# Performance work log

Hardware: AMD Instinct MI355X
Metric: run time of the kernel (lower is better)

The kernel has to match this reference:

```python
import jax, jax.numpy as jnp
import numpy as np

B, L, D = 2, 4096, 128      # batch, seq_len, d_model
ED = 2 * D                  # d_inner (expand=2) = 256
N = 16                      # d_state
K = 4                       # d_conv
R = (D + 15) // 16          # dt_rank = 8
H = 2 * D                   # mlp hidden = 256


def setup_inputs() -> dict:
    key = jax.random.key(0)
    ks = jax.random.split(key, 20)
    s = 0.05
    inp = {
        "x": jax.random.normal(ks[0], (B, L, D), dtype=jnp.float32),
        # outer block LayerNorm (norm1)
        "norm1_g": jnp.ones((D,), jnp.float32),
        "norm1_b": jnp.zeros((D,), jnp.float32),
        # MambaLayer inner LayerNorm
        "inner_g": jnp.ones((D,), jnp.float32),
        "inner_b": jnp.zeros((D,), jnp.float32),
        # Mamba params
        "in_w": jax.random.normal(ks[1], (2 * ED, D), jnp.float32) * s,      # in_proj (no bias)
        "conv_w": jax.random.normal(ks[2], (ED, 1, K), jnp.float32) * s,     # depthwise conv
        "conv_b": jax.random.normal(ks[3], (ED,), jnp.float32) * s,
        "xproj_w": jax.random.normal(ks[4], (R + 2 * N, ED), jnp.float32) * s,  # x_proj (no bias)
        "dt_w": jax.random.normal(ks[5], (ED, R), jnp.float32) * s,
        "dt_b": jax.random.normal(ks[6], (ED,), jnp.float32) * s,
        "A_log": jnp.tile(jnp.log(jnp.arange(1, N + 1, dtype=jnp.float32)), (ED, 1)),  # [ED,N]
        "Dp": jnp.ones((ED,), jnp.float32),
        "out_w": jax.random.normal(ks[7], (D, ED), jnp.float32) * s,         # out_proj (no bias)
        # MLP
        "fc1_w": jax.random.normal(ks[8], (H, D), jnp.float32) * s,
        "fc1_b": jnp.zeros((H,), jnp.float32),
        "fc2_w": jax.random.normal(ks[9], (D, H), jnp.float32) * s,
        "fc2_b": jnp.zeros((D,), jnp.float32),
    }
    return inp


def _ln(x, g, b, eps=1e-5):
    m = jnp.mean(x, axis=-1, keepdims=True)
    v = jnp.mean((x - m) ** 2, axis=-1, keepdims=True)
    return (x - m) * jax.lax.rsqrt(v + eps) * g + b


def _mamba(x, in_w, conv_w, conv_b, xproj_w, dt_w, dt_b, A_log, Dp, out_w):
    # x: [B, L, D]
    xz = jnp.einsum('bld,ed->ble', x, in_w)          # [B,L,2*ED]
    u, z = jnp.split(xz, 2, axis=-1)                 # each [B,L,ED]
    # causal depthwise conv1d over L
    u_c = jnp.transpose(u, (0, 2, 1))                # [B,ED,L]
    u_c = jax.lax.conv_general_dilated(
        u_c, conv_w, window_strides=(1,), padding=[(K - 1, 0)],
        dimension_numbers=('NCH', 'OIH', 'NCH'), feature_group_count=ED)
    u = jax.nn.silu(jnp.transpose(u_c, (0, 2, 1)) + conv_b)   # [B,L,ED]
    # input-dependent dt, B, C
    dbc = jnp.einsum('ble,re->blr', u, xproj_w)      # [B,L,R+2N]
    dt, Bm, Cm = jnp.split(dbc, [R, R + N], axis=-1)
    delta = jax.nn.softplus(jnp.einsum('blr,er->ble', dt, dt_w) + dt_b)  # [B,L,ED]
    A = -jnp.exp(A_log)                              # [ED,N]
    deltaA = jnp.exp(jnp.einsum('ble,en->blen', delta, A))               # [B,L,ED,N]
    deltaBu = jnp.einsum('ble,bln,ble->blen', delta, Bm, u)              # [B,L,ED,N]
    # selective scan over L
    def step(h, inp):
        dA, dBu, Ct = inp                            # [B,ED,N],[B,ED,N],[B,N]
        h = dA * h + dBu
        y = jnp.einsum('ben,bn->be', h, Ct)
        return h, y
    h0 = jnp.zeros((B, ED, N), u.dtype)
    xs = (jnp.transpose(deltaA, (1, 0, 2, 3)),
          jnp.transpose(deltaBu, (1, 0, 2, 3)),
          jnp.transpose(Cm, (1, 0, 2)))
    _, ys = jax.lax.scan(step, h0, xs)               # [L,B,ED]
    y = jnp.transpose(ys, (1, 0, 2)) + u * Dp        # [B,L,ED]
    y = y * jax.nn.silu(z)
    return jnp.einsum('ble,de->bld', y, out_w)       # [B,L,D]


def reference(x, norm1_g, norm1_b, inner_g, inner_b, in_w, conv_w, conv_b,
              xproj_w, dt_w, dt_b, A_log, Dp, out_w, fc1_w, fc1_b, fc2_w, fc2_b):
    # attn branch: mamba(inner_LN(norm1(x)))
    a = _mamba(_ln(_ln(x, norm1_g, norm1_b), inner_g, inner_b),
               in_w, conv_w, conv_b, xproj_w, dt_w, dt_b, A_log, Dp, out_w)
    x = x + a
    # mlp branch (note: original applies norm1 again to updated x)
    h = _ln(x, norm1_g, norm1_b)
    h = jax.nn.gelu(jnp.einsum('bld,hd->blh', h, fc1_w) + fc1_b, approximate=False)
    h = jnp.einsum('blh,dh->bld', h, fc2_w) + fc2_b
    return x + h
```

## Files before the change

kernel.cpp:

```cpp
#include <hip/hip_runtime.h>
#include <hip/hip_bf16.h>
#include <math.h>

#define BB 2
#define LL 4096
#define DD 128
#define ED 256
#define NN 16
#define KK 4
#define RR 8
#define HH 256
#define NT (BB*LL)
#define NC 128
#define LC 32

#define LOG2E 1.4426950408889634f

typedef __attribute__((ext_vector_type(8))) short short8;
typedef __attribute__((ext_vector_type(8))) unsigned short ushort8v;
typedef __attribute__((ext_vector_type(4))) float floatx4;

__device__ __forceinline__ unsigned short f2bf(float f) {
  unsigned int b = __builtin_bit_cast(unsigned int, f);
  b += 0x7FFFu + ((b >> 16) & 1u);
  return (unsigned short)(b >> 16);
}

__device__ __forceinline__ float exp2_fast(float x) {
#if __has_builtin(__builtin_amdgcn_exp2f)
  return __builtin_amdgcn_exp2f(x);
#else
  return exp2f(x);
#endif
}

__device__ __forceinline__ ushort8v pack8(const float4& v0, const float4& v1) {
  ushort8v p;
  p[0]=f2bf(v0.x); p[1]=f2bf(v0.y); p[2]=f2bf(v0.z); p[3]=f2bf(v0.w);
  p[4]=f2bf(v1.x); p[5]=f2bf(v1.y); p[6]=f2bf(v1.z); p[7]=f2bf(v1.w);
  return p;
}

__global__ __launch_bounds__(256) void scan1g_k(
    const float* __restrict__ x,
    const float* __restrict__ g1, const float* __restrict__ b1,
    const float* __restrict__ g2, const float* __restrict__ b2,
    const float* __restrict__ in_w,
    const float* __restrict__ cw, const float* __restrict__ cb,
    const float* __restrict__ xpw,
    const float* __restrict__ dtw, const float* __restrict__ dtb,
    const float* __restrict__ A_log,
    float* __restrict__ uc, float* __restrict__ dbc,
    float* __restrict__ delta, float* __restrict__ gate,
    float* __restrict__ cA, float* __restrict__ cH) {
  __shared__ __align__(16) unsigned char SM[69776];
  auto Atile = reinterpret_cast<unsigned short(*)[136]>(SM);
  auto Wch   = reinterpret_cast<unsigned short(*)[136]>(SM);
  auto As    = reinterpret_cast<unsigned short(*)[264]>(SM);
  auto sdel  = reinterpret_cast<float(*)[128]>(SM);
  auto ubuf  = reinterpret_cast<float(*)[257]>(SM + 17408);
  auto Bs    = reinterpret_cast<unsigned short(*)[264]>(SM + 17408);
  auto sdbc  = reinterpret_cast<float(*)[40]>(SM + 17408);
  auto sus   = reinterpret_cast<float(*)[128]>(SM + 53392);

  const int eb = blockIdx.x, c = blockIdx.y, b = blockIdx.z;
  const int tid = threadIdx.x;
  const int t0 = b*LL + c*LC;
  const int wave = tid >> 6, lane = tid & 63;
  const int quad = lane >> 4, l16 = lane & 15;

  {
    const int lr = tid >> 2, lk = (tid & 3) * 32;
    if (lr < 48) {
      if (lr < 35 && !(c == 0 && lr < 3)) {
        const float* Ap = x + (size_t)(t0 - 3 + lr)*DD + lk;
        float4 av[8];
        float s = 0.f, sq = 0.f;
        #pragma unroll
        for (int g = 0; g < 8; g++) {
          av[g] = *(const float4*)(Ap + g*4);
          s  += av[g].x + av[g].y + av[g].z + av[g].w;
          sq += av[g].x*av[g].x + av[g].y*av[g].y + av[g].z*av[g].z + av[g].w*av[g].w;
        }
        s += __shfl_xor(s, 1);  s += __shfl_xor(s, 2);
        sq += __shfl_xor(sq, 1); sq += __shfl_xor(sq, 2);
        const float m1 = s * (1.f/128.f);
        const float rs1 = rsqrtf(sq*(1.f/128.f) - m1*m1 + 1e-5f);
        float s2 = 0.f, sq2 = 0.f;
        #pragma unroll
        for (int g = 0; g < 8; g++) {
          const float4 gg = *(const float4*)(g1 + lk + g*4);
          const float4 bb = *(const float4*)(b1 + lk + g*4);
          av[g].x = (av[g].x - m1)*rs1*gg.x + bb.x;
          av[g].y = (av[g].y - m1)*rs1*gg.y + bb.y;
          av[g].z = (av[g].z - m1)*rs1*gg.z + bb.z;
          av[g].w = (av[g].w - m1)*rs1*gg.w + bb.w;
          s2  += av[g].x + av[g].y + av[g].z + av[g].w;
          sq2 += av[g].x*av[g].x + av[g].y*av[g].y + av[g].z*av[g].z + av[g].w*av[g].w;
        }
        s2 += __shfl_xor(s2, 1);  s2 += __shfl_xor(s2, 2);
        sq2 += __shfl_xor(sq2, 1); sq2 += __shfl_xor(sq2, 2);
        const float m2 = s2 * (1.f/128.f);
        const float rs2 = rsqrtf(sq2*(1.f/128.f) - m2*m2 + 1e-5f);
        #pragma unroll
        for (int g = 0; g < 4; g++) {
          const float4 ga = *(const float4*)(g2 + lk + g*8);
          const float4 gb = *(const float4*)(g2 + lk + g*8 + 4);
          const float4 ba = *(const float4*)(b2 + lk + g*8);
          const float4 bbv= *(const float4*)(b2 + lk + g*8 + 4);
          ushort8v pa;
          pa[0] = f2bf((av[2*g].x   - m2)*rs2*ga.x + ba.x);
          pa[1] = f2bf((av[2*g].y   - m2)*rs2*ga.y + ba.y);
          pa[2] = f2bf((av[2*g].z   - m2)*rs2*ga.z + ba.z);
          pa[3] = f2bf((av[2*g].w   - m2)*rs2*ga.w + ba.w);
          pa[4] = f2bf((av[2*g+1].x - m2)*rs2*gb.x + bbv.x);
          pa[5] = f2bf((av[2*g+1].y - m2)*rs2*gb.y + bbv.y);
          pa[6] = f2bf((av[2*g+1].z - m2)*rs2*gb.z + bbv.z);
          pa[7] = f2bf((av[2*g+1].w - m2)*rs2*gb.w + bbv.w);
          *(ushort8v*)&Atile[lr][lk + g*8] = pa;
        }
      } else {
        const ushort8v zz = {};
        #pragma unroll
        for (int g = 0; g < 4; g++) *(ushort8v*)&Atile[lr][lk + g*8] = zz;
      }
    }
  }
  __syncthreads();

  short8 af[3][4];
  #pragma unroll
  for (int mt = 0; mt < 3; mt++)
    #pragma unroll
    for (int ks = 0; ks < 4; ks++)
      af[mt][ks] = *(const short8*)&Atile[mt*16 + l16][ks*32 + quad*8];
  __syncthreads();

  for (int nc = 0; nc < 6; nc++) {
    const int colbase = (nc < 4) ? nc*64 : 256 + eb*128 + (nc-4)*64;
    {
      const int r = tid >> 2, seg = (tid & 3) * 32;
      const float* wp = in_w + (size_t)(colbase + r)*DD + seg;
      #pragma unroll
      for (int g = 0; g < 4; g++) {
        const float4 v0 = *(const float4*)(wp + g*8);
        const float4 v1 = *(const float4*)(wp + g*8 + 4);
        *(ushort8v*)&Wch[r][seg + g*8] = pack8(v0, v1);
      }
    }
    __syncthreads();
    floatx4 acc[3] = {};
    #pragma unroll
    for (int ks = 0; ks < 4; ks++) {
      short8 bv = *(const short8*)&Wch[wave*16 + l16][ks*32 + quad*8];
      #pragma unroll
      for (int mt = 0; mt < 3; mt++)
        acc[mt] = __builtin_amdgcn_mfma_f32_16x16x32_bf16(af[mt][ks], bv, acc[mt], 0, 0, 0);
    }
    const int coll = wave*16 + l16;
    #pragma unroll
    for (int mt = 0; mt < 3; mt++)
      #pragma unroll
      for (int rr = 0; rr < 4; rr++) {
        const int m = mt*16 + quad*4 + rr;
        if (nc < 4) {
          if (m < 35) ubuf[m][nc*64 + coll] = acc[mt][rr];
        } else {
          if (m >= 3 && m < 35) {
            const float v = acc[mt][rr];
            gate[(size_t)(t0 + m - 3)*ED + (colbase - 256) + coll] =
                v / (1.f + __expf(-v));
          }
        }
      }
    __syncthreads();
  }

  {
    const int ch = tid;
    const float4 w = *(const float4*)(cw + ch*4);
    const float cbe = cb[ch];
    float h0 = ubuf[0][ch], h1 = ubuf[1][ch], h2 = ubuf[2][ch];
    const bool own = (ch >> 7) == eb;
    #pragma unroll
    for (int i = 0; i < LC; i++) {
      const float cur = ubuf[3+i][ch];
      const float a = cbe + h0*w.x + h1*w.y + h2*w.z + cur*w.w;
      const float s = a / (1.f + __expf(-a));
      As[i][ch] = f2bf(s);
      if (own) {
        sus[i][ch & 127] = s;
        uc[(size_t)(t0+i)*ED + ch] = s;
      }
      h0 = h1; h1 = h2; h2 = cur;
    }
  }
  __syncthreads();

  #pragma unroll
  for (int p = 0; p < 8; p++) {
    const int idx = p*256 + tid;
    const int row = idx >> 5;
    const int col = (idx & 31) * 8;
    ushort8v v = {};
    if (row < 40) {
      const float4 v0 = *(const float4*)(xpw + (size_t)row*ED + col);
      const float4 v1 = *(const float4*)(xpw + (size_t)row*ED + col + 4);
      v = pack8(v0, v1);
    }
    *(ushort8v*)&Bs[row][col] = v;
  }
  __syncthreads();

  {
    const int mi = (wave & 1) * 16;
    const int j0 = (wave >> 1) * 2;
    floatx4 acc[2] = {};
    #pragma unroll
    for (int ks = 0; ks < 8; ks++) {
      const int ko = ks*32 + quad*8;
      short8 a  = *(const short8*)&As[mi + l16][ko];
      short8 b0 = *(const short8*)&Bs[j0*16 +      l16][ko];
      short8 b1 = *(const short8*)&Bs[j0*16 + 16 + l16][ko];
      acc[0] = __builtin_amdgcn_mfma_f32_16x16x32_bf16(a, b0, acc[0], 0, 0, 0);
      acc[1] = __builtin_amdgcn_mfma_f32_16x16x32_bf16(a, b1, acc[1], 0, 0, 0);
    }
    __syncthreads();
    #pragma unroll
    for (int f = 0; f < 2; f++) {
      const int n = (j0 + f)*16 + l16;
      #pragma unroll
      for (int r = 0; r < 4; r++) {
        const int m = mi + quad*4 + r;
        if (n < 40) {
          sdbc[m][n] = acc[f][r];
          if (eb == 0) dbc[(size_t)(t0 + m)*40 + n] = acc[f][r];
        }
      }
    }
  }
  __syncthreads();

  const int e_loc = tid >> 1;
  const int half  = tid & 1;
  const int e     = eb*128 + e_loc;
  {
    const float4 w0 = *(const float4*)(dtw + e*RR);
    const float4 w1 = *(const float4*)(dtw + e*RR + 4);
    const float db = dtb[e];
    #pragma unroll 4
    for (int i = 0; i < 16; i++) {
      const int t = half*16 + i;
      const float a = db
          + sdbc[t][0]*w0.x + sdbc[t][1]*w0.y + sdbc[t][2]*w0.z + sdbc[t][3]*w0.w
          + sdbc[t][4]*w1.x + sdbc[t][5]*w1.y + sdbc[t][6]*w1.z + sdbc[t][7]*w1.w;
      const float d = (a > 20.f) ? a : log1pf(__expf(a));
      sdel[t][e_loc] = d;
      delta[(size_t)(t0+t)*ED + e] = d;
    }
  }
  __syncthreads();

  const int n0 = half * 8;
  const float4 a0 = *(const float4*)(A_log + e*NN + n0);
  const float4 a1 = *(const float4*)(A_log + e*NN + n0 + 4);
  float Aen[8] = {-__expf(a0.x)*LOG2E, -__expf(a0.y)*LOG2E,
                  -__expf(a0.z)*LOG2E, -__expf(a0.w)*LOG2E,
                  -__expf(a1.x)*LOG2E, -__expf(a1.y)*LOG2E,
                  -__expf(a1.z)*LOG2E, -__expf(a1.w)*LOG2E};
  float h[8] = {};
  float sumd = 0.f;
  for (int i = 0; i < LC; i++) {
    const float dv = sdel[i][e_loc];
    const float du = dv * sus[i][e_loc];
    const float4 B0 = *(const float4*)&sdbc[i][RR + n0];
    const float4 B1 = *(const float4*)&sdbc[i][RR + n0 + 4];
    const float Bv[8] = {B0.x,B0.y,B0.z,B0.w,B1.x,B1.y,B1.z,B1.w};
    sumd += dv;
    #pragma unroll
    for (int j = 0; j < 8; j++)
      h[j] = exp2_fast(dv * Aen[j])*h[j] + Bv[j]*du;
  }
  const size_t base = (((size_t)c*BB + b)*ED + e)*NN + n0;
  *(float4*)(cA + base)     = make_float4(exp2_fast(sumd*Aen[0]), exp2_fast(sumd*Aen[1]),
                                          exp2_fast(sumd*Aen[2]), exp2_fast(sumd*Aen[3]));
  *(float4*)(cA + base + 4) = make_float4(exp2_fast(sumd*Aen[4]), exp2_fast(sumd*Aen[5]),
                                          exp2_fast(sumd*Aen[6]), exp2_fast(sumd*Aen[7]));
  *(float4*)(cH + base)     = make_float4(h[0], h[1], h[2], h[3]);
  *(float4*)(cH + base + 4) = make_float4(h[4], h[5], h[6], h[7]);
}

__global__ __launch_bounds__(64) void scan2_k(float* __restrict__ cA,
    const float* __restrict__ cH) {
  const int gt = blockIdx.x*64 + threadIdx.x;
  const int b = gt >> 12;
  const size_t base = (size_t)b*ED*NN + (gt & 4095);
  float h = 0.f;
  for (int g = 0; g < NC/16; g++) {
    float av[16], hv[16];
    #pragma unroll
    for (int i = 0; i < 16; i++) {
      const size_t idx = (size_t)(g*16 + i)*(BB*ED*NN) + base;
      av[i] = cA[idx]; hv[i] = cH[idx];
    }
    #pragma unroll
    for (int i = 0; i < 16; i++) {
      const size_t idx = (size_t)(g*16 + i)*(BB*ED*NN) + base;
      cA[idx] = h;
      h = av[i]*h + hv[i];
    }
  }
}

__global__ __launch_bounds__(512, 1) void tail6_k(
    const float* __restrict__ gate, const float* __restrict__ delta,
    const float* __restrict__ uc, const float* __restrict__ dbc,
    const float* __restrict__ cP, const float* __restrict__ A_log,
    const float* __restrict__ Dpv, const float* __restrict__ x,
    const float* __restrict__ g1, const float* __restrict__ b1,
    const float* __restrict__ out_w, const float* __restrict__ fc1_w,
    const float* __restrict__ fc1_b, const float* __restrict__ fc2_w,
    const float* __restrict__ fc2_b, float* __restrict__ out) {
  __shared__ __align__(16) unsigned short BigW[34816];
  __shared__ __align__(16) unsigned short Au[32][264];
  __shared__ float xs[32][132];
  __shared__ float sbc[32][32];

  const int c = blockIdx.x, b = blockIdx.y;
  const int t0 = b*LL + c*LC;
  const int tid = threadIdx.x;
  const int wave = tid >> 6, lane = tid & 63;
  const int quad = lane >> 4, l16 = lane & 15;

  if (tid < 256) {
    const int row = tid >> 3, c4 = (tid & 7) * 4;
    *(float4*)&sbc[row][c4] = *(const float4*)(dbc + (size_t)(t0 + row)*40 + RR + c4);
  }
  __syncthreads();

  {
    const int r = tid >> 2, k0 = (tid & 3) * 64;
    const float* wp = out_w + (size_t)r*ED + k0;
    #pragma unroll
    for (int g = 0; g < 8; g++) {
      const float4 v0 = *(const float4*)(wp + g*8);
      const float4 v1 = *(const float4*)(wp + g*8 + 4);
      *(ushort8v*)&BigW[(size_t)r*264 + k0 + g*8] = pack8(v0, v1);
    }
  }

  {
    const int e = tid >> 1, half = tid & 1;
    const int n0 = half * 8;
    float Aen[8], h[8];
    {
      const float4 a0 = *(const float4*)(A_log + e*NN + n0);
      const float4 a1 = *(const float4*)(A_log + e*NN + n0 + 4);
      Aen[0]=-__expf(a0.x)*LOG2E; Aen[1]=-__expf(a0.y)*LOG2E;
      Aen[2]=-__expf(a0.z)*LOG2E; Aen[3]=-__expf(a0.w)*LOG2E;
      Aen[4]=-__expf(a1.x)*LOG2E; Aen[5]=-__expf(a1.y)*LOG2E;
      Aen[6]=-__expf(a1.z)*LOG2E; Aen[7]=-__expf(a1.w)*LOG2E;
      const size_t pb = (((size_t)c*BB + b)*ED + e)*NN + n0;
      const float4 h0 = *(const float4*)(cP + pb);
      const float4 h1 = *(const float4*)(cP + pb + 4);
      h[0]=h0.x; h[1]=h0.y; h[2]=h0.z; h[3]=h0.w;
      h[4]=h1.x; h[5]=h1.y; h[6]=h1.z; h[7]=h1.w;
    }
    const float Dpe = Dpv[e];
    float pd[8], pu[8], pg[8];
    #pragma unroll
    for (int i = 0; i < 8; i++) {
      pd[i] = delta[(size_t)(t0+i)*ED + e];
      pu[i] = uc[(size_t)(t0+i)*ED + e];
      pg[i] = gate[(size_t)(t0+i)*ED + e];
    }
    for (int g4 = 0; g4 < 4; g4++) {
      float cd[8], cu[8], cg[8];
      #pragma unroll
      for (int i = 0; i < 8; i++) { cd[i]=pd[i]; cu[i]=pu[i]; cg[i]=pg[i]; }
      if (g4 < 3) {
        const int tn = t0 + (g4+1)*8;
        #pragma unroll
        for (int i = 0; i < 8; i++) {
          pd[i] = delta[(size_t)(tn+i)*ED + e];
          pu[i] = uc[(size_t)(tn+i)*ED + e];
          pg[i] = gate[(size_t)(tn+i)*ED + e];
        }
      }
      #pragma unroll
      for (int i = 0; i < 8; i++) {
        const int t = g4*8 + i;
        const float dv = cd[i];
        const float uv = cu[i];
        const float du = dv * uv;
        const float4 B0 = *(const float4*)&sbc[t][n0];
        const float4 B1 = *(const float4*)&sbc[t][n0 + 4];
        const float4 C0 = *(const float4*)&sbc[t][16 + n0];
        const float4 C1 = *(const float4*)&sbc[t][16 + n0 + 4];
        const float Bv[8] = {B0.x,B0.y,B0.z,B0.w, B1.x,B1.y,B1.z,B1.w};
        const float Cv[8] = {C0.x,C0.y,C0.z,C0.w, C1.x,C1.y,C1.z,C1.w};
        float part = 0.f;
        #pragma unroll
        for (int j = 0; j < 8; j++) {
          h[j] = exp2_fast(dv * Aen[j])*h[j] + Bv[j]*du;
          part += h[j]*Cv[j];
        }
        part += __shfl_xor(part, 1);
        if (half == 0)
          Au[t][e] = f2bf((part + uv*Dpe) * cg[i]);
      }
    }
  }
  __syncthreads();

  {
    const int wn = wave * 16;
    floatx4 acc[2] = {};
    #pragma unroll
    for (int ks = 0; ks < 8; ks++) {
      const int ko = ks*32 + quad*8;
      short8 a0 = *(const short8*)&Au[l16][ko];
      short8 a1 = *(const short8*)&Au[16 + l16][ko];
      short8 bv = *(const short8*)&BigW[(size_t)(wn + l16)*264 + ko];
      acc[0] = __builtin_amdgcn_mfma_f32_16x16x32_bf16(a0, bv, acc[0], 0, 0, 0);
      acc[1] = __builtin_amdgcn_mfma_f32_16x16x32_bf16(a1, bv, acc[1], 0, 0, 0);
    }
    #pragma unroll
    for (int i = 0; i < 2; i++) {
      const int n = wn + l16;
      #pragma unroll
      for (int r = 0; r < 4; r++) {
        const int m = i*16 + quad*4 + r;
        xs[m][n] = acc[i][r] + x[(size_t)(t0 + m)*DD + n];
      }
    }
  }
  __syncthreads();

  {
    const int lr = tid >> 4, le = (tid & 15) * 8;
    float vv[8];
    float s = 0.f, sq = 0.f;
    #pragma unroll
    for (int i = 0; i < 8; i++) {
      vv[i] = xs[lr][le + i];
      s += vv[i]; sq += vv[i]*vv[i];
    }
    s += __shfl_xor(s, 1);  s += __shfl_xor(s, 2);
    s += __shfl_xor(s, 4);  s += __shfl_xor(s, 8);
    sq += __shfl_xor(sq, 1); sq += __shfl_xor(sq, 2);
    sq += __shfl_xor(sq, 4); sq += __shfl_xor(sq, 8);
    const float mean = s * (1.f/128.f);
    const float rs = rsqrtf(sq*(1.f/128.f) - mean*mean + 1e-5f);
    ushort8v p;
    #pragma unroll
    for (int i = 0; i < 8; i++)
      p[i] = f2bf((vv[i] - mean)*rs*g1[le + i] + b1[le + i]);
    *(ushort8v*)&Au[lr][le] = p;
  }
  {
    const int r = tid >> 1, k0 = (tid & 1) * 64;
    const float* wp = fc1_w + (size_t)r*DD + k0;
    #pragma unroll
    for (int g = 0; g < 8; g++) {
      const float4 v0 = *(const float4*)(wp + g*8);
      const float4 v1 = *(const float4*)(wp + g*8 + 4);
      *(ushort8v*)&BigW[(size_t)r*136 + k0 + g*8] = pack8(v0, v1);
    }
  }
  __syncthreads();

  {
    const int wn = wave * 32;
    floatx4 acc[2][2] = {};
    #pragma unroll
    for (int ks = 0; ks < 4; ks++) {
      const int ko = ks*32 + quad*8;
      short8 a0 = *(const short8*)&Au[l16][ko];
      short8 a1 = *(const short8*)&Au[16 + l16][ko];
      short8 b0 = *(const short8*)&BigW[(size_t)(wn +      l16)*136 + ko];
      short8 b1 = *(const short8*)&BigW[(size_t)(wn + 16 + l16)*136 + ko];
      acc[0][0] = __builtin_amdgcn_mfma_f32_16x16x32_bf16(a0, b0, acc[0][0], 0, 0, 0);
      acc[0][1] = __builtin_amdgcn_mfma_f32_16x16x32_bf16(a0, b1, acc[0][1], 0, 0, 0);
      acc[1][0] = __builtin_amdgcn_mfma_f32_16x16x32_bf16(a1, b0, acc[1][0], 0, 0, 0);
      acc[1][1] = __builtin_amdgcn_mfma_f32_16x16x32_bf16(a1, b1, acc[1][1], 0, 0, 0);
    }
    __syncthreads();
    #pragma unroll
    for (int i = 0; i < 2; i++)
      #pragma unroll
      for (int f = 0; f < 2; f++) {
        const int n = wn + f*16 + l16;
        const float bn = fc1_b[n];
        #pragma unroll
        for (int r = 0; r < 4; r++) {
          const int m = i*16 + quad*4 + r;
          float v = acc[i][f][r] + bn;
          v = 0.5f*v*(1.f + erff(v*0.70710678118f));
          Au[m][n] = f2bf(v);
        }
      }
  }
  {
    const int r = tid >> 2, k0 = (tid & 3) * 64;
    const float* wp = fc2_w + (size_t)r*HH + k0;
    __syncthreads();
    #pragma unroll
    for (int g = 0; g < 8; g++) {
      const float4 v0 = *(const float4*)(wp + g*8);
      const float4 v1 = *(const float4*)(wp + g*8 + 4);
      *(ushort8v*)&BigW[(size_t)r*264 + k0 + g*8] = pack8(v0, v1);
    }
  }
  __syncthreads();

  {
    const int wn = wave * 16;
    floatx4 acc[2] = {};
    #pragma unroll
    for (int ks = 0; ks < 8; ks++) {
      const int ko = ks*32 + quad*8;
      short8 a0 = *(const short8*)&Au[l16][ko];
      short8 a1 = *(const short8*)&Au[16 + l16][ko];
      short8 bv = *(const short8*)&BigW[(size_t)(wn + l16)*264 + ko];
      acc[0] = __builtin_amdgcn_mfma_f32_16x16x32_bf16(a0, bv, acc[0], 0, 0, 0);
      acc[1] = __builtin_amdgcn_mfma_f32_16x16x32_bf16(a1, bv, acc[1], 0, 0, 0);
    }
    #pragma unroll
    for (int i = 0; i < 2; i++) {
      const int n = wn + l16;
      const float bn = fc2_b[n];
      #pragma unroll
      for (int r = 0; r < 4; r++) {
        const int m = i*16 + quad*4 + r;
        out[(size_t)(t0 + m)*DD + n] = acc[i][r] + bn + xs[m][n];
      }
    }
  }
}

extern "C" void kernel_launch(void* const* d_in, const int* in_sizes, int n_in,
                              void* d_out, int out_size, void* d_ws, size_t ws_size,
                              hipStream_t stream) {
  const float* x      = (const float*)d_in[0];
  const float* n1g    = (const float*)d_in[1];
  const float* n1b    = (const float*)d_in[2];
  const float* ing    = (const float*)d_in[3];
  const float* inb    = (const float*)d_in[4];
  const float* in_w   = (const float*)d_in[5];
  const float* conv_w = (const float*)d_in[6];
  const float* conv_b = (const float*)d_in[7];
  const float* xproj_w= (const float*)d_in[8];
  const float* dt_w   = (const float*)d_in[9];
  const float* dt_b   = (const float*)d_in[10];
  const float* A_log  = (const float*)d_in[11];
  const float* Dpv    = (const float*)d_in[12];
  const float* out_w  = (const float*)d_in[13];
  const float* fc1_w  = (const float*)d_in[14];
  const float* fc1_b  = (const float*)d_in[15];
  const float* fc2_w  = (const float*)d_in[16];
  const float* fc2_b  = (const float*)d_in[17];
  float* out = (float*)d_out;

  float* ws    = (float*)d_ws;
  float* uc    = ws;
  float* dbc   = uc    + (size_t)NT*ED;
  float* delta = dbc   + (size_t)NT*40;
  float* gate  = delta + (size_t)NT*ED;
  float* cA    = gate  + (size_t)NT*ED;
  float* cH    = cA    + (size_t)NC*BB*ED*NN;

  scan1g_k<<<dim3(2, NC, BB), 256, 0, stream>>>(x, n1g, n1b, ing, inb, in_w,
                                                conv_w, conv_b, xproj_w, dt_w, dt_b,
                                                A_log, uc, dbc, delta, gate, cA, cH);
  scan2_k<<<(BB*ED*NN)/64, 64, 0, stream>>>(cA, cH);
  tail6_k<<<dim3(NC, BB), 512, 0, stream>>>(gate, delta, uc, dbc, cA, A_log, Dpv,
                                            x, n1g, n1b, out_w, fc1_w, fc1_b,
                                            fc2_w, fc2_b, out);
}
```

Measured before the change: 164.5 us.

## Parallelize chunk-carry scan into four segments and double tail kernel threads

The inter-chunk carry scan now splits each of the 8192 state scans across four threads. Each thread composes the affine transform over its 32 chunks, the prefixes are combined with lane shuffles, and then each segment rewrites its carries, so the serial chain is shorter and there are four times more threads. The tail kernel moves from 512 to 1024 threads: each thread handles 4 state dims instead of 8, and the out_proj, fc1 and fc2 MFMA tiles are split across twice as many waves. The cost is that the scan reads cA/cH twice, and the larger block may raise register pressure or limit occupancy.

Measured after the change: 166.0 us. About the same (+0.9%).

```diff
diff --git a/kernel.cpp b/kernel.cpp
--- a/kernel.cpp
+++ b/kernel.cpp
@@ -290,29 +290,55 @@
   *(float4*)(cH + base + 4) = make_float4(h[4], h[5], h[6], h[7]);
 }
 
-__global__ __launch_bounds__(64) void scan2_k(float* __restrict__ cA,
+__global__ __launch_bounds__(256) void scan2p_k(float* __restrict__ cA,
     const float* __restrict__ cH) {
-  const int gt = blockIdx.x*64 + threadIdx.x;
-  const int b = gt >> 12;
-  const size_t base = (size_t)b*ED*NN + (gt & 4095);
+  const int gt = blockIdx.x*256 + threadIdx.x;
+  const int scan = gt >> 2;
+  const int seg  = gt & 3;
+  const int lane = threadIdx.x & 63;
+  const int lb   = lane & ~3;
+  const int b = scan >> 12;
+  const size_t base = (size_t)b*ED*NN + (scan & 4095);
+  const int c0 = seg * 32;
+
+  float ap = 1.f, hs = 0.f;
+  for (int g = 0; g < 2; g++) {
+    float av[16], hv[16];
+    #pragma unroll
+    for (int i = 0; i < 16; i++) {
+      const size_t idx = (size_t)(c0 + g*16 + i)*(BB*ED*NN) + base;
+      av[i] = cA[idx]; hv[i] = cH[idx];
+    }
+    #pragma unroll
+    for (int i = 0; i < 16; i++) {
+      hs = av[i]*hs + hv[i];
+      ap *= av[i];
+    }
+  }
   float h = 0.f;
-  for (int g = 0; g < NC/16; g++) {
+  #pragma unroll
+  for (int k = 0; k < 3; k++) {
+    const float ak = __shfl(ap, lb + k);
+    const float hk = __shfl(hs, lb + k);
+    if (seg > k) h = ak*h + hk;
+  }
+  for (int g = 0; g < 2; g++) {
     float av[16], hv[16];
     #pragma unroll
     for (int i = 0; i < 16; i++) {
-      const size_t idx = (size_t)(g*16 + i)*(BB*ED*NN) + base;
+      const size_t idx = (size_t)(c0 + g*16 + i)*(BB*ED*NN) + base;
       av[i] = cA[idx]; hv[i] = cH[idx];
     }
     #pragma unroll
     for (int i = 0; i < 16; i++) {
-      const size_t idx = (size_t)(g*16 + i)*(BB*ED*NN) + base;
+      const size_t idx = (size_t)(c0 + g*16 + i)*(BB*ED*NN) + base;
       cA[idx] = h;
       h = av[i]*h + hv[i];
     }
   }
 }
 
-__global__ __launch_bounds__(512, 1) void tail6_k(
+__global__ __launch_bounds__(1024) void tail7_k(
     const float* __restrict__ gate, const float* __restrict__ delta,
     const float* __restrict__ uc, const float* __restrict__ dbc,
     const float* __restrict__ cP, const float* __restrict__ A_log,
@@ -339,10 +365,10 @@
   __syncthreads();
 
   {
-    const int r = tid >> 2, k0 = (tid & 3) * 64;
+    const int r = tid >> 3, k0 = (tid & 7) * 32;
     const float* wp = out_w + (size_t)r*ED + k0;
     #pragma unroll
-    for (int g = 0; g < 8; g++) {
+    for (int g = 0; g < 4; g++) {
       const float4 v0 = *(const float4*)(wp + g*8);
       const float4 v1 = *(const float4*)(wp + g*8 + 4);
       *(ushort8v*)&BigW[(size_t)r*264 + k0 + g*8] = pack8(v0, v1);
@@ -350,21 +376,15 @@
   }
 
   {
-    const int e = tid >> 1, half = tid & 1;
-    const int n0 = half * 8;
-    float Aen[8], h[8];
+    const int e = tid >> 2, q = tid & 3;
+    const int n0 = q * 4;
+    float Aen[4], h[4];
     {
       const float4 a0 = *(const float4*)(A_log + e*NN + n0);
-      const float4 a1 = *(const float4*)(A_log + e*NN + n0 + 4);
       Aen[0]=-__expf(a0.x)*LOG2E; Aen[1]=-__expf(a0.y)*LOG2E;
       Aen[2]=-__expf(a0.z)*LOG2E; Aen[3]=-__expf(a0.w)*LOG2E;
-      Aen[4]=-__expf(a1.x)*LOG2E; Aen[5]=-__expf(a1.y)*LOG2E;
-      Aen[6]=-__expf(a1.z)*LOG2E; Aen[7]=-__expf(a1.w)*LOG2E;
-      const size_t pb = (((size_t)c*BB + b)*ED + e)*NN + n0;
-      const float4 h0 = *(const float4*)(cP + pb);
-      const float4 h1 = *(const float4*)(cP + pb + 4);
+      const float4 h0 = *(const float4*)(cP + (((size_t)c*BB + b)*ED + e)*NN + n0);
       h[0]=h0.x; h[1]=h0.y; h[2]=h0.z; h[3]=h0.w;
-      h[4]=h1.x; h[5]=h1.y; h[6]=h1.z; h[7]=h1.w;
     }
     const float Dpe = Dpv[e];
     float pd[8], pu[8], pg[8];
@@ -394,19 +414,18 @@
         const float uv = cu[i];
         const float du = dv * uv;
         const float4 B0 = *(const float4*)&sbc[t][n0];
-        const float4 B1 = *(const float4*)&sbc[t][n0 + 4];
         const float4 C0 = *(const float4*)&sbc[t][16 + n0];
-        const float4 C1 = *(const float4*)&sbc[t][16 + n0 + 4];
-        const float Bv[8] = {B0.x,B0.y,B0.z,B0.w, B1.x,B1.y,B1.z,B1.w};
-        const float Cv[8] = {C0.x,C0.y,C0.z,C0.w, C1.x,C1.y,C1.z,C1.w};
+        const float Bv[4] = {B0.x,B0.y,B0.z,B0.w};
+        const float Cv[4] = {C0.x,C0.y,C0.z,C0.w};
         float part = 0.f;
         #pragma unroll
-        for (int j = 0; j < 8; j++) {
+        for (int j = 0; j < 4; j++) {
           h[j] = exp2_fast(dv * Aen[j])*h[j] + Bv[j]*du;
           part += h[j]*Cv[j];
         }
         part += __shfl_xor(part, 1);
-        if (half == 0)
+        part += __shfl_xor(part, 2);
+        if (q == 0)
           Au[t][e] = f2bf((part + uv*Dpe) * cg[i]);
       }
     }
@@ -414,30 +433,26 @@
   __syncthreads();
 
   {
-    const int wn = wave * 16;
-    floatx4 acc[2] = {};
+    const int mi = (wave & 1) * 16;
+    const int wn = (wave >> 1) * 16;
+    floatx4 acc = {};
     #pragma unroll
     for (int ks = 0; ks < 8; ks++) {
       const int ko = ks*32 + quad*8;
-      short8 a0 = *(const short8*)&Au[l16][ko];
-      short8 a1 = *(const short8*)&Au[16 + l16][ko];
+      short8 a  = *(const short8*)&Au[mi + l16][ko];
       short8 bv = *(const short8*)&BigW[(size_t)(wn + l16)*264 + ko];
-      acc[0] = __builtin_amdgcn_mfma_f32_16x16x32_bf16(a0, bv, acc[0], 0, 0, 0);
-      acc[1] = __builtin_amdgcn_mfma_f32_16x16x32_bf16(a1, bv, acc[1], 0, 0, 0);
-    }
-    #pragma unroll
-    for (int i = 0; i < 2; i++) {
-      const int n = wn + l16;
-      #pragma unroll
-      for (int r = 0; r < 4; r++) {
-        const int m = i*16 + quad*4 + r;
-        xs[m][n] = acc[i][r] + x[(size_t)(t0 + m)*DD + n];
-      }
-    }
-  }
-  __syncthreads();
-
-  {
+      acc = __builtin_amdgcn_mfma_f32_16x16x32_bf16(a, bv, acc, 0, 0, 0);
+    }
+    const int n = wn + l16;
+    #pragma unroll
+    for (int r = 0; r < 4; r++) {
+      const int m = mi + quad*4 + r;
+      xs[m][n] = acc[r] + x[(size_t)(t0 + m)*DD + n];
+    }
+  }
+  __syncthreads();
+
+  if (tid < 512) {
     const int lr = tid >> 4, le = (tid & 15) * 8;
     float vv[8];
     float s = 0.f, sq = 0.f;
@@ -459,10 +474,10 @@
     *(ushort8v*)&Au[lr][le] = p;
   }
   {
-    const int r = tid >> 1, k0 = (tid & 1) * 64;
+    const int r = tid >> 2, k0 = (tid & 3) * 32;
     const float* wp = fc1_w + (size_t)r*DD + k0;
     #pragma unroll
-    for (int g = 0; g < 8; g++) {
+    for (int g = 0; g < 4; g++) {
       const float4 v0 = *(const float4*)(wp + g*8);
       const float4 v1 = *(const float4*)(wp + g*8 + 4);
       *(ushort8v*)&BigW[(size_t)r*136 + k0 + g*8] = pack8(v0, v1);
@@ -471,42 +486,37 @@
   __syncthreads();
 
   {
-    const int wn = wave * 32;
-    floatx4 acc[2][2] = {};
+    const int mi = (wave & 1) * 16;
+    const int wn = (wave >> 1) * 32;
+    floatx4 acc[2] = {};
     #pragma unroll
     for (int ks = 0; ks < 4; ks++) {
       const int ko = ks*32 + quad*8;
-      short8 a0 = *(const short8*)&Au[l16][ko];
-      short8 a1 = *(const short8*)&Au[16 + l16][ko];
+      short8 a  = *(const short8*)&Au[mi + l16][ko];
       short8 b0 = *(const short8*)&BigW[(size_t)(wn +      l16)*136 + ko];
       short8 b1 = *(const short8*)&BigW[(size_t)(wn + 16 + l16)*136 + ko];
-      acc[0][0] = __builtin_amdgcn_mfma_f32_16x16x32_bf16(a0, b0, acc[0][0], 0, 0, 0);
-      acc[0][1] = __builtin_amdgcn_mfma_f32_16x16x32_bf16(a0, b1, acc[0][1], 0, 0, 0);
-      acc[1][0] = __builtin_amdgcn_mfma_f32_16x16x32_bf16(a1, b0, acc[1][0], 0, 0, 0);
-      acc[1][1] = __builtin_amdgcn_mfma_f32_16x16x32_bf16(a1, b1, acc[1][1], 0, 0, 0);
+      acc[0] = __builtin_amdgcn_mfma_f32_16x16x32_bf16(a, b0, acc[0], 0, 0, 0);
+      acc[1] = __builtin_amdgcn_mfma_f32_16x16x32_bf16(a, b1, acc[1], 0, 0, 0);
     }
     __syncthreads();
     #pragma unroll
-    for (int i = 0; i < 2; i++)
-      #pragma unroll
-      for (int f = 0; f < 2; f++) {
-        const int n = wn + f*16 + l16;
-        const float bn = fc1_b[n];
-        #pragma unroll
-        for (int r = 0; r < 4; r++) {
-          const int m = i*16 + quad*4 + r;
-          float v = acc[i][f][r] + bn;
-          v = 0.5f*v*(1.f + erff(v*0.70710678118f));
-          Au[m][n] = f2bf(v);
-        }
-      }
-  }
-  {
-    const int r = tid >> 2, k0 = (tid & 3) * 64;
+    for (int f = 0; f < 2; f++) {
+      const int n = wn + f*16 + l16;
+      const float bn = fc1_b[n];
+      #pragma unroll
+      for (int r = 0; r < 4; r++) {
+        const int m = mi + quad*4 + r;
+        float v = acc[f][r] + bn;
+        v = 0.5f*v*(1.f + erff(v*0.70710678118f));
+        Au[m][n] = f2bf(v);
+      }
+    }
+  }
+  {
+    const int r = tid >> 3, k0 = (tid & 7) * 32;
     const float* wp = fc2_w + (size_t)r*HH + k0;
-    __syncthreads();
-    #pragma unroll
-    for (int g = 0; g < 8; g++) {
+    #pragma unroll
+    for (int g = 0; g < 4; g++) {
       const float4 v0 = *(const float4*)(wp + g*8);
       const float4 v1 = *(const float4*)(wp + g*8 + 4);
       *(ushort8v*)&BigW[(size_t)r*264 + k0 + g*8] = pack8(v0, v1);
@@ -515,26 +525,22 @@
   __syncthreads();
 
   {
-    const int wn = wave * 16;
-    floatx4 acc[2] = {};
+    const int mi = (wave & 1) * 16;
+    const int wn = (wave >> 1) * 16;
+    floatx4 acc = {};
     #pragma unroll
     for (int ks = 0; ks < 8; ks++) {
       const int ko = ks*32 + quad*8;
-      short8 a0 = *(const short8*)&Au[l16][ko];
-      short8 a1 = *(const short8*)&Au[16 + l16][ko];
+      short8 a  = *(const short8*)&Au[mi + l16][ko];
       short8 bv = *(const short8*)&BigW[(size_t)(wn + l16)*264 + ko];
-      acc[0] = __builtin_amdgcn_mfma_f32_16x16x32_bf16(a0, bv, acc[0], 0, 0, 0);
-      acc[1] = __builtin_amdgcn_mfma_f32_16x16x32_bf16(a1, bv, acc[1], 0, 0, 0);
-    }
-    #pragma unroll
-    for (int i = 0; i < 2; i++) {
-      const int n = wn + l16;
-      const float bn = fc2_b[n];
-      #pragma unroll
-      for (int r = 0; r < 4; r++) {
-        const int m = i*16 + quad*4 + r;
-        out[(size_t)(t0 + m)*DD + n] = acc[i][r] + bn + xs[m][n];
-      }
+      acc = __builtin_amdgcn_mfma_f32_16x16x32_bf16(a, bv, acc, 0, 0, 0);
+    }
+    const int n = wn + l16;
+    const float bn = fc2_b[n];
+    #pragma unroll
+    for (int r = 0; r < 4; r++) {
+      const int m = mi + quad*4 + r;
+      out[(size_t)(t0 + m)*DD + n] = acc[r] + bn + xs[m][n];
     }
   }
 }
@@ -573,8 +579,8 @@
   scan1g_k<<<dim3(2, NC, BB), 256, 0, stream>>>(x, n1g, n1b, ing, inb, in_w,
                                                 conv_w, conv_b, xproj_w, dt_w, dt_b,
                                                 A_log, uc, dbc, delta, gate, cA, cH);
-  scan2_k<<<(BB*ED*NN)/64, 64, 0, stream>>>(cA, cH);
-  tail6_k<<<dim3(NC, BB), 512, 0, stream>>>(gate, delta, uc, dbc, cA, A_log, Dpv,
-                                            x, n1g, n1b, out_w, fc1_w, fc1_b,
-                                            fc2_w, fc2_b, out);
-}
+  scan2p_k<<<(4*BB*ED*NN)/256, 256, 0, stream>>>(cA, cH);
+  tail7_k<<<dim3(NC, BB), 1024, 0, stream>>>(gate, delta, uc, dbc, cA, A_log, Dpv,
+                                             x, n1g, n1b, out_w, fc1_w, fc1_b,
+                                             fc2_w, fc2_b, out);
+}
```
